# Performance work log

Hardware: AMD Instinct MI355X
Metric: run time of the kernel (lower is better)

## Reference

```python
import jax, jax.numpy as jnp
import numpy as np

K = 20          # args.k
NEG = 0.2       # LeakyReLU negative slope

def lrelu(x):
    return jnp.where(x >= 0, x, NEG * x)

def bn(x, s, b):
    # eval-mode batchnorm folded into per-channel affine; channel axis = 1
    sh = (1, -1) + (1,) * (x.ndim - 2)
    return x * s.reshape(sh) + b.reshape(sh)

def se(x, w1, w2):
    # Squeeze-and-Excite on (B, C, N, k)
    y = jnp.mean(x, axis=(2, 3))                      # (B, C)
    y = jax.nn.sigmoid(jax.nn.relu(y @ w1.T) @ w2.T)  # (B, C)
    return x * y[:, :, None, None]

def graph_feature(x):
    # x: (B, C, N) -> edge features (B, 2C, N, K)
    xx = jnp.sum(x * x, axis=1)                        # (B, N)
    inner = jnp.einsum('bcn,bcm->bnm', x, x)           # (B, N, N)
    dist = -xx[:, :, None] + 2.0 * inner - xx[:, None, :]
    idx = jax.lax.top_k(dist, K)[1]                    # (B, N, K) nearest (incl. self)
    xt = jnp.transpose(x, (0, 2, 1))                   # (B, N, C)
    nbr = jax.vmap(lambda t, i: t[i])(xt, idx)         # (B, N, K, C)
    ctr = xt[:, :, None, :]
    out = jnp.concatenate([nbr - ctr, jnp.broadcast_to(ctr, nbr.shape)], axis=3)
    return jnp.transpose(out, (0, 3, 1, 2))

def edge_block(x, w, s, b, w1, w2):
    # get_graph_feature -> 1x1 conv -> BN -> SE -> LeakyReLU -> max over k
    g = graph_feature(x)                               # (B, 2C, N, K)
    h = jnp.einsum('bcnk,oc->bonk', g, w)
    h = lrelu(se(bn(h, s, b), w1, w2))
    return jnp.max(h, axis=-1)                         # (B, O, N)

def forward(x, conv1_w, conv2_w, conv3_w, conv4_w, conv5_w,
            bn1_s, bn1_b, bn2_s, bn2_b, bn3_s, bn3_b, bn4_s, bn4_b, bn5_s, bn5_b,
            se1_w1, se1_w2, se2_w1, se2_w2, se3_w1, se3_w2, se4_w1, se4_w2,
            res1_w, res2_w, res3_w,
            lin1_w, bn6_s, bn6_b, lin2_w, lin2_b, bn7_s, bn7_b, lin3_w, lin3_b):
    x1 = edge_block(x, conv1_w, bn1_s, bn1_b, se1_w1, se1_w2)                 # (B,512,N)
    x2 = edge_block(x1, conv2_w, bn2_s, bn2_b, se2_w1, se2_w2)
    x2 = x2 + jnp.einsum('bcn,oc->bon', x1, res1_w)                           # (B,512,N)
    x3 = edge_block(x2, conv3_w, bn3_s, bn3_b, se3_w1, se3_w2)
    x3 = x3 + jnp.einsum('bcn,oc->bon', x2, res2_w)                           # (B,1024,N)
    x4 = edge_block(x3, conv4_w, bn4_s, bn4_b, se4_w1, se4_w2)
    x4 = x4 + jnp.einsum('bcn,oc->bon', x3, res3_w)                           # (B,1024,N)
    h = jnp.concatenate([x1, x2, x3, x4], axis=1)                             # (B,3072,N)
    h = lrelu(bn(jnp.einsum('bcn,oc->bon', h, conv5_w), bn5_s, bn5_b))        # (B,2048,N)
    f = jnp.concatenate([jnp.max(h, axis=-1), jnp.mean(h, axis=-1)], axis=1)  # (B,4096)
    f = lrelu(bn(f @ lin1_w.T, bn6_s, bn6_b))       # dropout is eval-mode identity
    f = lrelu(bn(f @ lin2_w.T + lin2_b, bn7_s, bn7_b))
    return f @ lin3_w.T + lin3_b                    # (B,40)

def setup_inputs():
    ks = jax.random.split(jax.random.key(0), 40)
    B, N = 16, 128
    f32 = jnp.float32
    def w(i, shape, s=0.02):
        return jax.random.normal(ks[i], shape, f32) * s
    def bns(i, c):
        return 1.0 + 0.1 * jax.random.normal(ks[i], (c,), f32)
    def bnb(i, c):
        return 0.1 * jax.random.normal(ks[i], (c,), f32)
    return {
        'x': jax.random.normal(ks[0], (B, 512, N), f32),
        'conv1_w': w(1, (512, 1024)),
        'conv2_w': w(2, (512, 1024)),
        'conv3_w': w(3, (1024, 1024)),
        'conv4_w': w(4, (1024, 2048)),
        'conv5_w': w(5, (2048, 3072)),
        'bn1_s': bns(6, 512), 'bn1_b': bnb(7, 512),
        'bn2_s': bns(8, 512), 'bn2_b': bnb(9, 512),
        'bn3_s': bns(10, 1024), 'bn3_b': bnb(11, 1024),
        'bn4_s': bns(12, 1024), 'bn4_b': bnb(13, 1024),
        'bn5_s': bns(14, 2048), 'bn5_b': bnb(15, 2048),
        'se1_w1': w(16, (32, 512), 0.05), 'se1_w2': w(17, (512, 32), 0.05),
        'se2_w1': w(18, (32, 512), 0.05), 'se2_w2': w(19, (512, 32), 0.05),
        'se3_w1': w(20, (64, 1024), 0.05), 'se3_w2': w(21, (1024, 64), 0.05),
        'se4_w1': w(22, (64, 1024), 0.05), 'se4_w2': w(23, (1024, 64), 0.05),
        'res1_w': w(24, (512, 512)),
        'res2_w': w(25, (1024, 512)),
        'res3_w': w(26, (1024, 1024)),
        'lin1_w': w(27, (512, 4096)),
        'bn6_s': bns(28, 512), 'bn6_b': bnb(29, 512),
        'lin2_w': w(30, (256, 512)), 'lin2_b': bnb(31, 256),
        'bn7_s': bns(32, 256), 'bn7_b': bnb(33, 256),
        'lin3_w': w(34, (40, 256)), 'lin3_b': bnb(35, 40),
    }

def reference(x, conv1_w, conv2_w, conv3_w, conv4_w, conv5_w,
              bn1_s, bn1_b, bn2_s, bn2_b, bn3_s, bn3_b, bn4_s, bn4_b, bn5_s, bn5_b,
              se1_w1, se1_w2, se2_w1, se2_w2, se3_w1, se3_w2, se4_w1, se4_w2,
              res1_w, res2_w, res3_w,
              lin1_w, bn6_s, bn6_b, lin2_w, lin2_b, bn7_s, bn7_b, lin3_w, lin3_b):
    return forward(x, conv1_w, conv2_w, conv3_w, conv4_w, conv5_w,
                   bn1_s, bn1_b, bn2_s, bn2_b, bn3_s, bn3_b, bn4_s, bn4_b, bn5_s, bn5_b,
                   se1_w1, se1_w2, se2_w1, se2_w2, se3_w1, se3_w2, se4_w1, se4_w2,
                   res1_w, res2_w, res3_w,
                   lin1_w, bn6_s, bn6_b, lin2_w, lin2_b, bn7_s, bn7_b, lin3_w, lin3_b)
```

## Files before the change

kernel.cpp:

```cpp
#include <hip/hip_runtime.h>
#include <hip/hip_bf16.h>


#define BN_ALL 2048
typedef __hip_bfloat16 bf16;
typedef __attribute__((ext_vector_type(8))) short short8;
typedef __attribute__((ext_vector_type(4))) float float4v;

__device__ __forceinline__ float b2f(bf16 v) { return __bfloat162float(v); }
__device__ __forceinline__ float lrelu(float v) { return v >= 0.f ? v : 0.2f * v; }
__device__ __forceinline__ short f2bs(float v) {
    bf16 h = __float2bfloat16(v);
    return *reinterpret_cast<short*>(&h);
}

__device__ __forceinline__ void gll16(const void* g, void* l) {
    __builtin_amdgcn_global_load_lds(
        (const __attribute__((address_space(1))) unsigned int*)g,
        (__attribute__((address_space(3))) unsigned int*)l,
        16, 0, 0);
}

__device__ __forceinline__ float ldin(const void* p, size_t i, int isb) {
    return isb ? __bfloat162float(((const bf16*)p)[i]) : ((const float*)p)[i];
}

__device__ __forceinline__ float ld1(const float* p) { return *p; }
__device__ __forceinline__ float ld1(const bf16* p)  { return __bfloat162float(*p); }
__device__ __forceinline__ void st1(float* p, float v) { *p = v; }
__device__ __forceinline__ void st1(bf16* p, float v)  { *p = __float2bfloat16(v); }
__device__ __forceinline__ short ldbs(const float* p) { return f2bs(*p); }
__device__ __forceinline__ short ldbs(const bf16* p)  { return *(const short*)p; }

__global__ __launch_bounds__(256) void detect_dtype(const void* __restrict__ x, int* __restrict__ flag) {
    const unsigned* u = (const unsigned*)x;
    int sane = 0;
    for (int i = threadIdx.x; i < 4096; i += 256) {
        unsigned e = (u[i] >> 23) & 0xFF;
        sane += (e >= 87 && e <= 167) ? 1 : 0;
    }
    __shared__ int sh[256];
    sh[threadIdx.x] = sane;
    __syncthreads();
    for (int off = 128; off > 0; off >>= 1) {
        if (threadIdx.x < off) sh[threadIdx.x] += sh[threadIdx.x + off];
        __syncthreads();
    }
    if (threadIdx.x == 0) *flag = (sh[0] < 2048) ? 1 : 0;
}

__global__ __launch_bounds__(256) void convert_kp(const void* __restrict__ x, bf16* __restrict__ X0,
                                                  const int* __restrict__ dflag) {
    int isb = *dflag;
    int item = blockIdx.x * 256 + threadIdx.x;
    int cg = item >> 11, bn = item & 2047;
    int b = bn >> 7, n = bn & 127;
    short8 pk;
#pragma unroll
    for (int j = 0; j < 8; ++j)
        pk[j] = f2bs(ldin(x, ((size_t)(b * 512 + cg * 8 + j)) * 128 + n, isb));
    *(short8*)((short*)X0 + ((size_t)cg * BN_ALL + bn) * 8) = pk;
}

__global__ __launch_bounds__(256) void gram_k(const bf16* __restrict__ X, int C,
                                              float* __restrict__ G) {
    __shared__ __align__(16) short Bsm[2][8192];
    int tid = threadIdx.x;
    int b = blockIdx.x;
    int lane = tid & 63, wv = tid >> 6, wm = wv & 1, wn = wv >> 1;
    int lq = lane >> 4, lr = lane & 15;
    int KC = C >> 6;
    const short* Xs = (const short*)X;

    float4v acc[4][4];
#pragma unroll
    for (int i = 0; i < 4; i++)
#pragma unroll
        for (int j = 0; j < 4; j++) acc[i][j] = (float4v){0.f, 0.f, 0.f, 0.f};

#pragma unroll
    for (int it = 0; it < 4; ++it) {
        int i = tid + it * 256;
        int q = i >> 7, c = i & 127;
        gll16(Xs + ((size_t)q * BN_ALL + b * 128 + c) * 8, &Bsm[0][(size_t)i * 8]);
    }
    __syncthreads();

    int p = 0;
    for (int kc = 0; kc < KC; ++kc) {
        if (kc + 1 < KC) {
#pragma unroll
            for (int it = 0; it < 4; ++it) {
                int i = tid + it * 256;
                int q = i >> 7, c = i & 127;
                gll16(Xs + ((size_t)((kc + 1) * 8 + q) * BN_ALL + b * 128 + c) * 8,
                      &Bsm[p ^ 1][(size_t)i * 8]);
            }
        }
#pragma unroll
        for (int h = 0; h < 2; ++h) {
            short8 av[4], bv[4];
#pragma unroll
            for (int mt = 0; mt < 4; ++mt)
                av[mt] = *(const short8*)&Bsm[p][(size_t)(h * 512 + (lq << 7) + wm * 64 + mt * 16 + lr) * 8];
#pragma unroll
            for (int nt = 0; nt < 4; ++nt)
                bv[nt] = *(const short8*)&Bsm[p][(size_t)(h * 512 + (lq << 7) + wn * 64 + nt * 16 + lr) * 8];
#pragma unroll
            for (int mt = 0; mt < 4; ++mt)
#pragma unroll
                for (int nt = 0; nt < 4; ++nt)
                    acc[mt][nt] = __builtin_amdgcn_mfma_f32_16x16x32_bf16(av[mt], bv[nt], acc[mt][nt], 0, 0, 0);
        }
        __syncthreads();
        p ^= 1;
    }

    float* Gb = G + (size_t)b * 16384;
#pragma unroll
    for (int mt = 0; mt < 4; ++mt)
#pragma unroll
        for (int r = 0; r < 4; ++r) {
            int row = wm * 64 + mt * 16 + lq * 4 + r;
#pragma unroll
            for (int nt = 0; nt < 4; ++nt) {
                int col = wn * 64 + nt * 16 + lr;
                Gb[row * 128 + col] = acc[mt][nt][r];
            }
        }
}

__global__ __launch_bounds__(256) void topk_k(const float* __restrict__ G, int* __restrict__ idx) {
    int gw = (blockIdx.x * 256 + threadIdx.x) >> 6;
    int lane = threadIdx.x & 63;
    int b = gw >> 7, n = gw & 127;
    const float* Gb = G + (size_t)b * 16384;
    float g0 = Gb[n * 128 + lane];
    float g1 = Gb[n * 128 + 64 + lane];
    float dnn = Gb[n * 129];
    float dm0 = Gb[lane * 129];
    float dm1 = Gb[(64 + lane) * 129];
    float d0 = 2.f * g0 - dnn - dm0;
    float d1 = 2.f * g1 - dnn - dm1;
#pragma unroll
    for (int k = 0; k < 20; ++k) {
        float v; int i;
        if (d1 > d0) { v = d1; i = 64 + lane; } else { v = d0; i = lane; }
#pragma unroll
        for (int off = 1; off < 64; off <<= 1) {
            float ov = __shfl_xor(v, off, 64);
            int   oi = __shfl_xor(i, off, 64);
            if (ov > v || (ov == v && oi < i)) { v = ov; i = oi; }
        }
        if (lane == 0) idx[gw * 20 + k] = i;
        if (i < 64) { if (lane == i) d0 = -3.0e38f; }
        else        { if (lane == i - 64) d1 = -3.0e38f; }
    }
}

template <typename S>
__global__ __launch_bounds__(128) void knn_topk(const S* __restrict__ X, int C, int* __restrict__ idx) {
    int b = blockIdx.x >> 7;
    int n = blockIdx.x & 127;
    int m = threadIdx.x;
    const S* base = X + b * 128;
    float s0 = 0, s1 = 0, q0 = 0, q1 = 0;
    for (int c = 0; c < C; c += 2) {
        const S* p = base + (size_t)c * BN_ALL;
        float xm0 = ld1(p + m),          xn0 = ld1(p + n);
        float xm1 = ld1(p + BN_ALL + m), xn1 = ld1(p + BN_ALL + n);
        s0 += xm0 * xn0; q0 += xm0 * xm0;
        s1 += xm1 * xn1; q1 += xm1 * xm1;
    }
    float inner = s0 + s1;
    float xxm   = q0 + q1;
    __shared__ float xx[128];
    __shared__ float dist[128];
    __shared__ float rv[128];
    __shared__ int   ri[128];
    xx[m] = xxm;
    __syncthreads();
    dist[m] = 2.0f * inner - xx[n] - xxm;
    for (int k = 0; k < 20; k++) {
        __syncthreads();
        rv[m] = dist[m]; ri[m] = m;
        __syncthreads();
        for (int off = 64; off > 0; off >>= 1) {
            if (m < off) {
                float a = rv[m], bv = rv[m + off];
                int ia = ri[m], ib = ri[m + off];
                if (bv > a || (bv == a && ib < ia)) { rv[m] = bv; ri[m] = ib; }
            }
            __syncthreads();
        }
        if (m == 0) { idx[blockIdx.x * 20 + k] = ri[0]; dist[ri[0]] = -3.0e38f; }
    }
}

__global__ __launch_bounds__(256) void pack_w(const void* __restrict__ w, int ldw,
                                              const void* __restrict__ res, int Cin, int O,
                                              int Mtot, int K, short* __restrict__ out,
                                              const int* __restrict__ dflag) {
    int isb = *dflag;
    int item = blockIdx.x * 256 + threadIdx.x;
    if (item >= Mtot * (K >> 3)) return;
    int m_local = item & 127;
    int rest = item >> 7;
    int q = rest & 3; rest >>= 2;
    int KC = K >> 5;
    int kc = rest % KC, tm = rest / KC;
    int grow = tm * 128 + m_local;
    int k = kc * 32 + q * 8;
    const void* src; size_t base; int dif = 0;
    if (grow < O)          { src = w;   base = (size_t)grow * ldw + k; }
    else if (grow < 2 * O) { src = w;   base = (size_t)(grow - O) * ldw + k; dif = 1; }
    else                   { src = res; base = (size_t)(grow - 2 * O) * Cin + k; }
    short8 pk;
#pragma unroll
    for (int j = 0; j < 8; ++j) {
        float v = ldin(src, base + j, isb);
        if (dif) v = ldin(src, base + Cin + j, isb) - v;
        pk[j] = f2bs(v);
    }
    *(short8*)&out[(size_t)item * 8] = pk;
}

__global__ __launch_bounds__(256) void gemm_pk(const short* __restrict__ packA,
                                               const bf16* __restrict__ X, float* __restrict__ Cm, int K,
                                               const void* __restrict__ bnS, const void* __restrict__ bnB,
                                               int act, const int* __restrict__ dflag) {
    __shared__ __align__(16) short Asm[2][8192];
    __shared__ __align__(16) short Bsm[2][4096];
    int tid = threadIdx.x;
    int bm  = blockIdx.x << 7;
    int bn0 = blockIdx.y << 6;
    int lane = tid & 63, wv = tid >> 6, wm = wv & 1, wn = wv >> 1;
    int lq = lane >> 4, lr = lane & 15;
    int KC = K >> 6;
    const short* abase = packA + (size_t)blockIdx.x * (K >> 5) * 4096;
    const short* Xs = (const short*)X;
    int bq = tid >> 6, bc = tid & 63;

    float4v acc[4][2];
#pragma unroll
    for (int i = 0; i < 4; i++)
#pragma unroll
        for (int j = 0; j < 2; j++) acc[i][j] = (float4v){0.f, 0.f, 0.f, 0.f};

#pragma unroll
    for (int it = 0; it < 4; ++it)
        gll16(abase + (size_t)(tid + it * 256) * 8, &Asm[0][(size_t)(tid + it * 256) * 8]);
    gll16(Xs + ((size_t)bq * BN_ALL + bn0 + bc) * 8,       &Bsm[0][(size_t)tid * 8]);
    gll16(Xs + ((size_t)(bq + 4) * BN_ALL + bn0 + bc) * 8, &Bsm[0][(size_t)(tid + 256) * 8]);
    __syncthreads();

    int p = 0;
    for (int kc = 0; kc < KC; ++kc) {
        if (kc + 1 < KC) {
            const short* ab = abase + (size_t)(kc + 1) * 8192;
#pragma unroll
            for (int it = 0; it < 4; ++it)
                gll16(ab + (size_t)(tid + it * 256) * 8, &Asm[p ^ 1][(size_t)(tid + it * 256) * 8]);
            gll16(Xs + ((size_t)((kc + 1) * 8 + bq) * BN_ALL + bn0 + bc) * 8,
                  &Bsm[p ^ 1][(size_t)tid * 8]);
            gll16(Xs + ((size_t)((kc + 1) * 8 + bq + 4) * BN_ALL + bn0 + bc) * 8,
                  &Bsm[p ^ 1][(size_t)(tid + 256) * 8]);
        }
#pragma unroll
        for (int h = 0; h < 2; ++h) {
            short8 av[4], bv[2];
#pragma unroll
            for (int mt = 0; mt < 4; ++mt)
                av[mt] = *(const short8*)&Asm[p][(size_t)(h * 512 + (lq << 7) + wm * 64 + mt * 16 + lr) * 8];
#pragma unroll
            for (int nt = 0; nt < 2; ++nt)
                bv[nt] = *(const short8*)&Bsm[p][(size_t)(h * 256 + (lq << 6) + wn * 32 + nt * 16 + lr) * 8];
#pragma unroll
            for (int mt = 0; mt < 4; ++mt)
#pragma unroll
                for (int nt = 0; nt < 2; ++nt)
                    acc[mt][nt] = __builtin_amdgcn_mfma_f32_16x16x32_bf16(av[mt], bv[nt], acc[mt][nt], 0, 0, 0);
        }
        __syncthreads();
        p ^= 1;
    }

    int isb = *dflag;
#pragma unroll
    for (int mt = 0; mt < 4; ++mt) {
#pragma unroll
        for (int r = 0; r < 4; ++r) {
            int row = bm + wm * 64 + mt * 16 + lq * 4 + r;
            float s = 1.f, bb = 0.f;
            if (bnS) { s = ldin(bnS, row, isb); bb = ldin(bnB, row, isb); }
#pragma unroll
            for (int nt = 0; nt < 2; ++nt) {
                int col = bn0 + wn * 32 + nt * 16 + lr;
                float v = acc[mt][nt][r];
                if (bnS) v = v * s + bb;
                if (act) v = lrelu(v);
                Cm[(size_t)row * BN_ALL + col] = v;
            }
        }
    }
}

template <typename S>
__global__ __launch_bounds__(256) void gemm_mfma(const void* __restrict__ w, int ldw,
                                                 const void* __restrict__ res, int Cin, int O,
                                                 const S* __restrict__ X, S* __restrict__ Cm, int K,
                                                 const void* __restrict__ bnS, const void* __restrict__ bnB,
                                                 int act, const int* __restrict__ dflag) {
    int isb = *dflag;
    __shared__ short Asm[4096];
    __shared__ short Bsm[4096];
    int tid = threadIdx.x;
    int bm  = blockIdx.x << 7;
    int bn0 = blockIdx.y << 7;
    int lane = tid & 63, wv = tid >> 6;
    int wm = wv & 1, wn = wv >> 1;
    int lq = lane >> 4, lr = lane & 15;

    float4v acc[4][4];
#pragma unroll
    for (int i = 0; i < 4; i++)
#pragma unroll
        for (int j = 0; j < 4; j++) acc[i][j] = (float4v){0.f, 0.f, 0.f, 0.f};

    for (int k0 = 0; k0 < K; k0 += 32) {
#pragma unroll
        for (int it = 0; it < 2; ++it) {
            int i = tid + it * 256;
            int m = i >> 2, q = i & 3;
            int grow = bm + m;
            const void* asrc; size_t abase; int dif = 0;
            if (grow < O)          { asrc = w;   abase = (size_t)grow * ldw; }
            else if (grow < 2 * O) { asrc = w;   abase = (size_t)(grow - O) * ldw; dif = 1; }
            else                   { asrc = res; abase = (size_t)(grow - 2 * O) * Cin; }
            size_t kk = (size_t)k0 + q * 8;
            short8 pk;
#pragma unroll
            for (int j = 0; j < 8; ++j) {
                float v = ldin(asrc, abase + kk + j, isb);
                if (dif) v = ldin(asrc, abase + Cin + kk + j, isb) - v;
                pk[j] = f2bs(v);
            }
            *(short8*)&Asm[(size_t)(q * 128 + m) * 8] = pk;
        }
#pragma unroll
        for (int it = 0; it < 2; ++it) {
            int i = tid + it * 256;
            int q = i >> 7, c = i & 127;
            const S* xp = X + (size_t)(k0 + q * 8) * BN_ALL + bn0 + c;
            short8 pk;
#pragma unroll
            for (int j = 0; j < 8; ++j) pk[j] = f2bs(ld1(xp + (size_t)j * BN_ALL));
            *(short8*)&Bsm[(size_t)i * 8] = pk;
        }
        __syncthreads();
        short8 av[4], bv[4];
#pragma unroll
        for (int mt = 0; mt < 4; ++mt)
            av[mt] = *(const short8*)&Asm[(size_t)((lq << 7) + wm * 64 + mt * 16 + lr) * 8];
#pragma unroll
        for (int nt = 0; nt < 4; ++nt)
            bv[nt] = *(const short8*)&Bsm[(size_t)((lq << 7) + wn * 64 + nt * 16 + lr) * 8];
#pragma unroll
        for (int mt = 0; mt < 4; ++mt)
#pragma unroll
            for (int nt = 0; nt < 4; ++nt)
                acc[mt][nt] = __builtin_amdgcn_mfma_f32_16x16x32_bf16(av[mt], bv[nt], acc[mt][nt], 0, 0, 0);
        __syncthreads();
    }
#pragma unroll
    for (int mt = 0; mt < 4; ++mt) {
#pragma unroll
        for (int r = 0; r < 4; ++r) {
            int row = bm + wm * 64 + mt * 16 + lq * 4 + r;
            float s = 1.f, bb = 0.f;
            if (bnS) { s = ldin(bnS, row, isb); bb = ldin(bnB, row, isb); }
#pragma unroll
            for (int nt = 0; nt < 4; ++nt) {
                int col = bn0 + wn * 64 + nt * 16 + lr;
                float v = acc[mt][nt][r];
                if (bnS) v = v * s + bb;
                if (act) v = lrelu(v);
                st1(Cm + (size_t)row * BN_ALL + col, v);
            }
        }
    }
}

template <typename S>
__global__ __launch_bounds__(256) void gather_pool(S* __restrict__ PS, const int* __restrict__ idx,
                                                   const void* __restrict__ bns, const void* __restrict__ bnb,
                                                   float* __restrict__ Mb, int O,
                                                   const int* __restrict__ dflag) {
    int isb = *dflag;
    int wv = threadIdx.x >> 6, lane = threadIdx.x & 63;
    int gw = blockIdx.x * 4 + wv;
    int o = gw >> 4, b = gw & 15;
    S* Prow = PS + (size_t)o * BN_ALL + b * 128;
    const S* Srow = PS + (size_t)(O + o) * BN_ALL + b * 128;
    int n0 = lane, n1 = lane + 64;
    const int* id0 = idx + (b * 128 + n0) * 20;
    const int* id1 = idx + (b * 128 + n1) * 20;
    float mx0 = -3.0e38f, mn0 = 3.0e38f, sm0 = 0.f;
    float mx1 = -3.0e38f, mn1 = 3.0e38f, sm1 = 0.f;
#pragma unroll
    for (int k = 0; k < 20; k++) {
        float p = ld1(Prow + id0[k]);
        mx0 = fmaxf(mx0, p); mn0 = fminf(mn0, p); sm0 += p;
    }
#pragma unroll
    for (int k = 0; k < 20; k++) {
        float p = ld1(Prow + id1[k]);
        mx1 = fmaxf(mx1, p); mn1 = fminf(mn1, p); sm1 += p;
    }
    float Sv0 = ld1(Srow + n0), Sv1 = ld1(Srow + n1);
    float s = ldin(bns, o, isb), bb = ldin(bnb, o, isb);
    float ext0 = (s >= 0.f) ? mx0 : mn0;
    float ext1 = (s >= 0.f) ? mx1 : mn1;
    float t0 = lrelu(s * (ext0 + Sv0) + bb);
    float t1 = lrelu(s * (ext1 + Sv1) + bb);
    st1(Prow + n0, t0);
    st1(Prow + n1, t1);
    float r1 = sm0 + sm1;
    float r2 = Sv0 + Sv1;
#pragma unroll
    for (int off = 32; off > 0; off >>= 1) {
        r1 += __shfl_xor(r1, off, 64);
        r2 += __shfl_xor(r2, off, 64);
    }
    if (lane == 0) Mb[b * O + o] = s * (r1 * (1.f / 2560.f) + r2 * (1.f / 128.f)) + bb;
}

__global__ __launch_bounds__(256) void se1_k(const float* __restrict__ Mb, const void* __restrict__ w1,
                                             float* __restrict__ Z, int O, int r,
                                             const int* __restrict__ dflag) {
    int isb = *dflag;
    int gw = (blockIdx.x * 256 + threadIdx.x) >> 6;
    int lane = threadIdx.x & 63;
    int b = gw / r, t = gw - b * r;
    const float* mv = Mb + (size_t)b * O;
    float acc = 0.f;
    for (int c = lane; c < O; c += 64) acc += ldin(w1, (size_t)t * O + c, isb) * mv[c];
#pragma unroll
    for (int off = 32; off > 0; off >>= 1) acc += __shfl_xor(acc, off, 64);
    if (lane == 0) Z[b * r + t] = fmaxf(acc, 0.f);
}

__global__ __launch_bounds__(256) void se2_k(const float* __restrict__ Z, const void* __restrict__ w2,
                                             float* __restrict__ Y, int O, int r,
                                             const int* __restrict__ dflag) {
    int isb = *dflag;
    int gw = (blockIdx.x * 256 + threadIdx.x) >> 6;
    int lane = threadIdx.x & 63;
    int b = gw / O, o = gw - b * O;
    float acc = 0.f;
    if (lane < r) acc = ldin(w2, (size_t)o * r + lane, isb) * Z[b * r + lane];
#pragma unroll
    for (int off = 32; off > 0; off >>= 1) acc += __shfl_xor(acc, off, 64);
    if (lane == 0) Y[b * O + o] = 1.f / (1.f + expf(-acc));
}

__global__ __launch_bounds__(256) void se_k(const float* __restrict__ Mb, const void* __restrict__ w1,
                                            const void* __restrict__ w2, float* __restrict__ Y, int O, int r,
                                            const int* __restrict__ dflag) {
    int isb = *dflag;
    int b = blockIdx.x, t = threadIdx.x;
    __shared__ float mloc[1024];
    __shared__ float z[64];
    for (int i = t; i < O; i += 256) mloc[i] = Mb[b * O + i];
    __syncthreads();
    if (t < r) {
        float acc = 0.f;
        for (int c = 0; c < O; c++) acc += ldin(w1, (size_t)t * O + c, isb) * mloc[c];
        z[t] = fmaxf(acc, 0.f);
    }
    __syncthreads();
    for (int o = t; o < O; o += 256) {
        float acc = 0.f;
        for (int j = 0; j < r; j++) acc += ldin(w2, (size_t)o * r + j, isb) * z[j];
        Y[b * O + o] = 1.f / (1.f + expf(-acc));
    }
}

__global__ __launch_bounds__(256) void finalize_kp(const float* __restrict__ PS, const float* __restrict__ Y,
                                                   int useR, bf16* __restrict__ Xdst, int O) {
    int item = blockIdx.x * 256 + threadIdx.x;
    int og = item >> 11, bn = item & 2047;
    int b = bn >> 7;
    short8 pk;
#pragma unroll
    for (int j = 0; j < 8; ++j) {
        int r = og * 8 + j;
        float v = Y[b * O + r] * PS[(size_t)r * BN_ALL + bn];
        if (useR) v += PS[(size_t)(2 * O + r) * BN_ALL + bn];
        pk[j] = f2bs(v);
    }
    *(short8*)((short*)Xdst + ((size_t)og * BN_ALL + bn) * 8) = pk;
}

template <typename SP, typename SD>
__global__ __launch_bounds__(256) void finalize(const SP* __restrict__ PS, const float* __restrict__ Y,
                                                int useR, SD* __restrict__ Xdst, int O) {
    int tid = blockIdx.x * 256 + threadIdx.x;
    int o = tid >> 11, bn = tid & 2047;
    int b = bn >> 7;
    float v = Y[b * O + o] * ld1(PS + tid);
    if (useR) v += ld1(PS + (size_t)(2 * O + o) * BN_ALL + bn);
    st1(Xdst + tid, v);
}

template <typename S>
__global__ __launch_bounds__(256) void convert_x(const void* __restrict__ x, S* __restrict__ X0,
                                                 const int* __restrict__ dflag) {
    int isb = *dflag;
    int tid = blockIdx.x * 256 + threadIdx.x;
    int c = tid >> 11, bn = tid & 2047;
    int b = bn >> 7, n = bn & 127;
    st1(X0 + tid, ldin(x, (size_t)(b * 512 + c) * 128 + n, isb));
}

template <typename S>
__global__ __launch_bounds__(256) void pool5(const S* __restrict__ H, float* __restrict__ f) {
    int wv = threadIdx.x >> 6, lane = threadIdx.x & 63;
    int gw = blockIdx.x * 4 + wv;
    int m = gw >> 4, b = gw & 15;
    const S* Hp = H + (size_t)m * BN_ALL + b * 128;
    float v0 = ld1(Hp + lane), v1 = ld1(Hp + 64 + lane);
    float mx = fmaxf(v0, v1);
    float sm = v0 + v1;
#pragma unroll
    for (int off = 32; off > 0; off >>= 1) {
        mx = fmaxf(mx, __shfl_xor(mx, off, 64));
        sm += __shfl_xor(sm, off, 64);
    }
    if (lane == 0) {
        f[b * 4096 + m] = mx;
        f[b * 4096 + 2048 + m] = sm * (1.f / 128.f);
    }
}

__global__ __launch_bounds__(256) void head_k(const float* __restrict__ in, const void* __restrict__ W,
                                              const void* __restrict__ bias, const void* __restrict__ bns,
                                              const void* __restrict__ bnb, float* __restrict__ outf,
                                              void* __restrict__ outb, int Kd, int Od, int act,
                                              const int* __restrict__ dflag) {
    int isb = *dflag;
    int gw = (blockIdx.x * 256 + threadIdx.x) >> 6;
    int lane = threadIdx.x & 63;
    if (gw >= 16 * Od) return;
    int b = gw / Od, o = gw - b * Od;
    const float* iv = in + b * Kd;
    float acc = 0.f;
    for (int k = lane; k < Kd; k += 64) acc += iv[k] * ldin(W, (size_t)o * Kd + k, isb);
    for (int off = 32; off > 0; off >>= 1) acc += __shfl_xor(acc, off, 64);
    if (lane == 0) {
        float v = acc;
        if (bias) v += ldin(bias, o, isb);
        if (bns) v = v * ldin(bns, o, isb) + ldin(bnb, o, isb);
        if (act) v = lrelu(v);
        if (outb) {
            if (isb) ((bf16*)outb)[gw] = __float2bfloat16(v);
            else     ((float*)outb)[gw] = v;
        } else outf[gw] = v;
    }
}

__global__ __launch_bounds__(256) void zero_out(bf16* o, int n) {
    int i = blockIdx.x * 256 + threadIdx.x;
    if (i < n) o[i] = __float2bfloat16(0.f);
}

#define UNPACK_INPUTS()                                                     \
    const void* x_in   = d_in[0];                                           \
    const void* conv1w = d_in[1];  const void* conv2w = d_in[2];            \
    const void* conv3w = d_in[3];  const void* conv4w = d_in[4];            \
    const void* conv5w = d_in[5];                                           \
    const void* bn1s = d_in[6],  * bn1b = d_in[7];                          \
    const void* bn2s = d_in[8],  * bn2b = d_in[9];                          \
    const void* bn3s = d_in[10], * bn3b = d_in[11];                         \
    const void* bn4s = d_in[12], * bn4b = d_in[13];                         \
    const void* bn5s = d_in[14], * bn5b = d_in[15];                         \
    const void* se1w1 = d_in[16], * se1w2 = d_in[17];                       \
    const void* se2w1 = d_in[18], * se2w2 = d_in[19];                       \
    const void* se3w1 = d_in[20], * se3w2 = d_in[21];                       \
    const void* se4w1 = d_in[22], * se4w2 = d_in[23];                       \
    const void* res1w = d_in[24]; const void* res2w = d_in[25];             \
    const void* res3w = d_in[26]; const void* lin1w = d_in[27];             \
    const void* bn6s = d_in[28], * bn6b = d_in[29];                         \
    const void* lin2w = d_in[30], * lin2b = d_in[31];                       \
    const void* bn7s = d_in[32], * bn7b = d_in[33];                         \
    const void* lin3w = d_in[34], * lin3b = d_in[35];

static void run_net_packed(void* const* d_in, void* d_out, void* d_ws, hipStream_t stream) {
    UNPACK_INPUTS();
    float* WS = (float*)d_ws;
    float* PS   = WS;
    bf16*  XC   = (bf16*)(WS + 6291456);
    short* PACK = (short*)(WS + 12582912);
    float* MB = WS + 15728640;
    float* YB = MB + 16384;
    float* FB = YB + 16384;
    float* F1 = FB + 65536;
    float* F2 = F1 + 8192;
    int* IDX  = (int*)(F2 + 4096);
    int* DFLAG = IDX + 40960;
    float* ZB = (float*)(DFLAG + 16);
    bf16*  X0 = (bf16*)(PS + (size_t)2048 * BN_ALL);
    float* GRAM = PS;
    bf16* X1 = XC;
    bf16* X2 = XC + (size_t)512 * BN_ALL;
    bf16* X3 = XC + (size_t)1024 * BN_ALL;
    bf16* X4 = XC + (size_t)2048 * BN_ALL;

    detect_dtype<<<1, 256, 0, stream>>>(x_in, DFLAG);
    convert_kp<<<512, 256, 0, stream>>>(x_in, X0, DFLAG);

    gram_k<<<16, 256, 0, stream>>>(X0, 512, GRAM);
    topk_k<<<512, 256, 0, stream>>>(GRAM, IDX);
    pack_w<<<256, 256, 0, stream>>>(conv1w, 1024, nullptr, 512, 512, 1024, 512, PACK, DFLAG);
    gemm_pk<<<dim3(8, 32), 256, 0, stream>>>(PACK, X0, PS, 512, nullptr, nullptr, 0, DFLAG);
    gather_pool<float><<<2048, 256, 0, stream>>>(PS, IDX, bn1s, bn1b, MB, 512, DFLAG);
    se1_k<<<128, 256, 0, stream>>>(MB, se1w1, ZB, 512, 32, DFLAG);
    se2_k<<<2048, 256, 0, stream>>>(ZB, se1w2, YB, 512, 32, DFLAG);
    finalize_kp<<<512, 256, 0, stream>>>(PS, YB, 0, X1, 512);

    gram_k<<<16, 256, 0, stream>>>(X1, 512, GRAM);
    topk_k<<<512, 256, 0, stream>>>(GRAM, IDX);
    pack_w<<<384, 256, 0, stream>>>(conv2w, 1024, res1w, 512, 512, 1536, 512, PACK, DFLAG);
    gemm_pk<<<dim3(12, 32), 256, 0, stream>>>(PACK, X1, PS, 512, nullptr, nullptr, 0, DFLAG);
    gather_pool<float><<<2048, 256, 0, stream>>>(PS, IDX, bn2s, bn2b, MB, 512, DFLAG);
    se1_k<<<128, 256, 0, stream>>>(MB, se2w1, ZB, 512, 32, DFLAG);
    se2_k<<<2048, 256, 0, stream>>>(ZB, se2w2, YB, 512, 32, DFLAG);
    finalize_kp<<<512, 256, 0, stream>>>(PS, YB, 1, X2, 512);

    gram_k<<<16, 256, 0, stream>>>(X2, 512, GRAM);
    topk_k<<<512, 256, 0, stream>>>(GRAM, IDX);
    pack_w<<<768, 256, 0, stream>>>(conv3w, 1024, res2w, 512, 1024, 3072, 512, PACK, DFLAG);
    gemm_pk<<<dim3(24, 32), 256, 0, stream>>>(PACK, X2, PS, 512, nullptr, nullptr, 0, DFLAG);
    gather_pool<float><<<4096, 256, 0, stream>>>(PS, IDX, bn3s, bn3b, MB, 1024, DFLAG);
    se1_k<<<256, 256, 0, stream>>>(MB, se3w1, ZB, 1024, 64, DFLAG);
    se2_k<<<4096, 256, 0, stream>>>(ZB, se3w2, YB, 1024, 64, DFLAG);
    finalize_kp<<<1024, 256, 0, stream>>>(PS, YB, 1, X3, 1024);

    gram_k<<<16, 256, 0, stream>>>(X3, 1024, GRAM);
    topk_k<<<512, 256, 0, stream>>>(GRAM, IDX);
    pack_w<<<1536, 256, 0, stream>>>(conv4w, 2048, res3w, 1024, 1024, 3072, 1024, PACK, DFLAG);
    gemm_pk<<<dim3(24, 32), 256, 0, stream>>>(PACK, X3, PS, 1024, nullptr, nullptr, 0, DFLAG);
    gather_pool<float><<<4096, 256, 0, stream>>>(PS, IDX, bn4s, bn4b, MB, 1024, DFLAG);
    se1_k<<<256, 256, 0, stream>>>(MB, se4w1, ZB, 1024, 64, DFLAG);
    se2_k<<<4096, 256, 0, stream>>>(ZB, se4w2, YB, 1024, 64, DFLAG);
    finalize_kp<<<1024, 256, 0, stream>>>(PS, YB, 1, X4, 1024);

    pack_w<<<3072, 256, 0, stream>>>(conv5w, 3072, nullptr, 3072, 2048, 2048, 3072, PACK, DFLAG);
    gemm_pk<<<dim3(16, 32), 256, 0, stream>>>(PACK, XC, PS, 3072, bn5s, bn5b, 1, DFLAG);
    pool5<float><<<8192, 256, 0, stream>>>(PS, FB);

    head_k<<<2048, 256, 0, stream>>>(FB, lin1w, nullptr, bn6s, bn6b, F1, nullptr, 4096, 512, 1, DFLAG);
    head_k<<<1024, 256, 0, stream>>>(F1, lin2w, lin2b, bn7s, bn7b, F2, nullptr, 512, 256, 1, DFLAG);
    head_k<<<160, 256, 0, stream>>>(F2, lin3w, lin3b, nullptr, nullptr, nullptr, d_out, 256, 40, 0, DFLAG);
}

template <typename S>
static void run_net(void* const* d_in, void* d_out, void* d_ws, hipStream_t stream) {
    UNPACK_INPUTS();
    const size_t RC = (size_t)3072 * BN_ALL;
    S* PS = (S*)d_ws;
    S* XC = PS + RC;
    S* X0 = PS + (size_t)2048 * BN_ALL;
    float* MB = (float*)(XC + RC);
    float* YB = MB + 16 * 1024;
    float* FB = YB + 16 * 1024;
    float* F1 = FB + 16 * 4096;
    float* F2 = F1 + 16 * 512;
    int* IDX  = (int*)(F2 + 16 * 256);
    int* DFLAG = IDX + 16 * 128 * 20;

    S* X1 = XC;
    S* X2 = XC + (size_t)512 * BN_ALL;
    S* X3 = XC + (size_t)1024 * BN_ALL;
    S* X4 = XC + (size_t)2048 * BN_ALL;

    detect_dtype<<<1, 256, 0, stream>>>(x_in, DFLAG);
    convert_x<S><<<4096, 256, 0, stream>>>(x_in, X0, DFLAG);

    knn_topk<S><<<2048, 128, 0, stream>>>(X0, 512, IDX);
    gemm_mfma<S><<<dim3(8, 16), 256, 0, stream>>>(conv1w, 1024, nullptr, 512, 512, X0, PS, 512, nullptr, nullptr, 0, DFLAG);
    gather_pool<S><<<2048, 256, 0, stream>>>(PS, IDX, bn1s, bn1b, MB, 512, DFLAG);
    se_k<<<16, 256, 0, stream>>>(MB, se1w1, se1w2, YB, 512, 32, DFLAG);
    finalize<S, S><<<4096, 256, 0, stream>>>(PS, YB, 0, X1, 512);

    knn_topk<S><<<2048, 128, 0, stream>>>(X1, 512, IDX);
    gemm_mfma<S><<<dim3(12, 16), 256, 0, stream>>>(conv2w, 1024, res1w, 512, 512, X1, PS, 512, nullptr, nullptr, 0, DFLAG);
    gather_pool<S><<<2048, 256, 0, stream>>>(PS, IDX, bn2s, bn2b, MB, 512, DFLAG);
    se_k<<<16, 256, 0, stream>>>(MB, se2w1, se2w2, YB, 512, 32, DFLAG);
    finalize<S, S><<<4096, 256, 0, stream>>>(PS, YB, 1, X2, 512);

    knn_topk<S><<<2048, 128, 0, stream>>>(X2, 512, IDX);
    gemm_mfma<S><<<dim3(24, 16), 256, 0, stream>>>(conv3w, 1024, res2w, 512, 1024, X2, PS, 512, nullptr, nullptr, 0, DFLAG);
    gather_pool<S><<<4096, 256, 0, stream>>>(PS, IDX, bn3s, bn3b, MB, 1024, DFLAG);
    se_k<<<16, 256, 0, stream>>>(MB, se3w1, se3w2, YB, 1024, 64, DFLAG);
    finalize<S, S><<<8192, 256, 0, stream>>>(PS, YB, 1, X3, 1024);

    knn_topk<S><<<2048, 128, 0, stream>>>(X3, 1024, IDX);
    gemm_mfma<S><<<dim3(24, 16), 256, 0, stream>>>(conv4w, 2048, res3w, 1024, 1024, X3, PS, 1024, nullptr, nullptr, 0, DFLAG);
    gather_pool<S><<<4096, 256, 0, stream>>>(PS, IDX, bn4s, bn4b, MB, 1024, DFLAG);
    se_k<<<16, 256, 0, stream>>>(MB, se4w1, se4w2, YB, 1024, 64, DFLAG);
    finalize<S, S><<<8192, 256, 0, stream>>>(PS, YB, 1, X4, 1024);

    gemm_mfma<S><<<dim3(16, 16), 256, 0, stream>>>(conv5w, 3072, nullptr, 3072, 2048, XC, PS, 3072, bn5s, bn5b, 1, DFLAG);
    pool5<S><<<8192, 256, 0, stream>>>(PS, FB);

    head_k<<<2048, 256, 0, stream>>>(FB, lin1w, nullptr, bn6s, bn6b, F1, nullptr, 4096, 512, 1, DFLAG);
    head_k<<<1024, 256, 0, stream>>>(F1, lin2w, lin2b, bn7s, bn7b, F2, nullptr, 512, 256, 1, DFLAG);
    head_k<<<160, 256, 0, stream>>>(F2, lin3w, lin3b, nullptr, nullptr, nullptr, d_out, 256, 40, 0, DFLAG);
}

extern "C" void kernel_launch(void* const* d_in, const int* in_sizes, int n_in,
                              void* d_out, int out_size, void* d_ws, size_t ws_size,
                              hipStream_t stream) {
    const size_t SMALL = (16 * 1024 + 16 * 1024 + 16 * 4096 + 16 * 512 + 16 * 256) * 4
                       + 16 * 128 * 20 * 4 + 8192;
    const size_t NEED_PACKED = (size_t)15728640 * 4 + SMALL;
    const size_t NEED_F32    = 2 * ((size_t)3072 * BN_ALL * 4) + SMALL;
    const size_t NEED_BF16   = 2 * ((size_t)3072 * BN_ALL * 2) + SMALL;
    if (ws_size >= NEED_PACKED) {
        run_net_packed(d_in, d_out, d_ws, stream);
    } else if (ws_size >= NEED_F32) {
        run_net<float>(d_in, d_out, d_ws, stream);
    } else if (ws_size >= NEED_BF16) {
        run_net<bf16>(d_in, d_out, d_ws, stream);
    } else {
        zero_out<<<3, 256, 0, stream>>>((bf16*)d_out, out_size);
    }
}
```

Before: 590.7 us.

## Add packed2 path fusing weight packing, topk with GEMM, and SE launches

Adds a new forward path used when the workspace is large enough. It packs every conv weight and converts the input in one launch up front. Each edge block runs its top-k selection and the packed-weight GEMM in a single grid so the two overlap, and the two SE matmuls are merged into one kernel. This removes many small launches and per-layer packing passes, at the cost of a larger workspace and heavier shared-memory use in the combined kernel.

```diff
diff --git a/kernel.cpp b/kernel.cpp
--- a/kernel.cpp
+++ b/kernel.cpp
@@ -29,8 +29,6 @@
 __device__ __forceinline__ float ld1(const bf16* p)  { return __bfloat162float(*p); }
 __device__ __forceinline__ void st1(float* p, float v) { *p = v; }
 __device__ __forceinline__ void st1(bf16* p, float v)  { *p = __float2bfloat16(v); }
-__device__ __forceinline__ short ldbs(const float* p) { return f2bs(*p); }
-__device__ __forceinline__ short ldbs(const bf16* p)  { return *(const short*)p; }
 
 __global__ __launch_bounds__(256) void detect_dtype(const void* __restrict__ x, int* __restrict__ flag) {
     const unsigned* u = (const unsigned*)x;
@@ -49,10 +47,9 @@
     if (threadIdx.x == 0) *flag = (sh[0] < 2048) ? 1 : 0;
 }
 
-__global__ __launch_bounds__(256) void convert_kp(const void* __restrict__ x, bf16* __restrict__ X0,
-                                                  const int* __restrict__ dflag) {
-    int isb = *dflag;
-    int item = blockIdx.x * 256 + threadIdx.x;
+__device__ __forceinline__ void convert_core(int bid, int tid, const void* __restrict__ x,
+                                             bf16* __restrict__ X0, int isb) {
+    int item = bid * 256 + tid;
     int cg = item >> 11, bn = item & 2047;
     int b = bn >> 7, n = bn & 127;
     short8 pk;
@@ -60,6 +57,62 @@
     for (int j = 0; j < 8; ++j)
         pk[j] = f2bs(ldin(x, ((size_t)(b * 512 + cg * 8 + j)) * 128 + n, isb));
     *(short8*)((short*)X0 + ((size_t)cg * BN_ALL + bn) * 8) = pk;
+}
+
+__global__ __launch_bounds__(256) void convert_kp(const void* __restrict__ x, bf16* __restrict__ X0,
+                                                  const int* __restrict__ dflag) {
+    convert_core(blockIdx.x, threadIdx.x, x, X0, *dflag);
+}
+
+__device__ __forceinline__ void pack_core(int item, int isb, const void* __restrict__ w, int ldw,
+                                          const void* __restrict__ res, int Cin, int O,
+                                          int Mtot, int K, short* __restrict__ out) {
+    if (item >= Mtot * (K >> 3)) return;
+    int m_local = item & 127;
+    int rest = item >> 7;
+    int q = rest & 3; rest >>= 2;
+    int KC = K >> 5;
+    int kc = rest % KC, tm = rest / KC;
+    int grow = tm * 128 + m_local;
+    int k = kc * 32 + q * 8;
+    const void* src; size_t base; int dif = 0;
+    if (grow < O)          { src = w;   base = (size_t)grow * ldw + k; }
+    else if (grow < 2 * O) { src = w;   base = (size_t)(grow - O) * ldw + k; dif = 1; }
+    else                   { src = res; base = (size_t)(grow - 2 * O) * Cin + k; }
+    short8 pk;
+#pragma unroll
+    for (int j = 0; j < 8; ++j) {
+        float v = ldin(src, base + j, isb);
+        if (dif) v = ldin(src, base + Cin + j, isb) - v;
+        pk[j] = f2bs(v);
+    }
+    *(short8*)&out[(size_t)item * 8] = pk;
+}
+
+__global__ __launch_bounds__(256) void pack_w(const void* __restrict__ w, int ldw,
+                                              const void* __restrict__ res, int Cin, int O,
+                                              int Mtot, int K, short* __restrict__ out,
+                                              const int* __restrict__ dflag) {
+    pack_core(blockIdx.x * 256 + threadIdx.x, *dflag, w, ldw, res, Cin, O, Mtot, K, out);
+}
+
+__global__ __launch_bounds__(256) void convert_pack_all(
+        const void* __restrict__ x, bf16* __restrict__ X0,
+        const void* __restrict__ w1c, const void* __restrict__ w2c, const void* __restrict__ w3c,
+        const void* __restrict__ w4c, const void* __restrict__ w5c,
+        const void* __restrict__ r1, const void* __restrict__ r2, const void* __restrict__ r3,
+        short* __restrict__ p1, short* __restrict__ p2, short* __restrict__ p3,
+        short* __restrict__ p4, short* __restrict__ p5,
+        const int* __restrict__ dflag) {
+    int isb = *dflag;
+    int bid = blockIdx.x, tid = threadIdx.x;
+    if (bid < 512) { convert_core(bid, tid, x, X0, isb); return; }
+    int pb = bid - 512;
+    if (pb < 256)       pack_core(pb * 256 + tid,          isb, w1c, 1024, nullptr, 512, 512, 1024, 512, p1);
+    else if (pb < 640)  pack_core((pb - 256) * 256 + tid,  isb, w2c, 1024, r1,      512, 512, 1536, 512, p2);
+    else if (pb < 1408) pack_core((pb - 640) * 256 + tid,  isb, w3c, 1024, r2,      512, 1024, 3072, 512, p3);
+    else if (pb < 2944) pack_core((pb - 1408) * 256 + tid, isb, w4c, 2048, r3,      1024, 1024, 3072, 1024, p4);
+    else                pack_core((pb - 2944) * 256 + tid, isb, w5c, 3072, nullptr, 3072, 2048, 2048, 3072, p5);
 }
 
 __global__ __launch_bounds__(256) void gram_k(const bf16* __restrict__ X, int C,
@@ -130,9 +183,10 @@
         }
 }
 
-__global__ __launch_bounds__(256) void topk_k(const float* __restrict__ G, int* __restrict__ idx) {
-    int gw = (blockIdx.x * 256 + threadIdx.x) >> 6;
-    int lane = threadIdx.x & 63;
+__device__ __forceinline__ void topk_core(int bid, int tid, const float* __restrict__ G,
+                                          int* __restrict__ idx) {
+    int gw = (bid * 256 + tid) >> 6;
+    int lane = tid & 63;
     int b = gw >> 7, n = gw & 127;
     const float* Gb = G + (size_t)b * 16384;
     float g0 = Gb[n * 128 + lane];
@@ -155,6 +209,109 @@
         if (lane == 0) idx[gw * 20 + k] = i;
         if (i < 64) { if (lane == i) d0 = -3.0e38f; }
         else        { if (lane == i - 64) d1 = -3.0e38f; }
+    }
+}
+
+__global__ __launch_bounds__(256) void topk_k(const float* __restrict__ G, int* __restrict__ idx) {
+    topk_core(blockIdx.x, threadIdx.x, G, idx);
+}
+
+__device__ __forceinline__ void gemm_core(int bx, int by, int tid,
+        const short* __restrict__ packA, const bf16* __restrict__ X,
+        float* __restrict__ Cm, int K,
+        const void* __restrict__ bnS, const void* __restrict__ bnB,
+        int act, const int* __restrict__ dflag) {
+    __shared__ __align__(16) short Asm[2][8192];
+    __shared__ __align__(16) short Bsm[2][4096];
+    int bm  = bx << 7;
+    int bn0 = by << 6;
+    int lane = tid & 63, wv = tid >> 6, wm = wv & 1, wn = wv >> 1;
+    int lq = lane >> 4, lr = lane & 15;
+    int KC = K >> 6;
+    const short* abase = packA + (size_t)bx * (K >> 5) * 4096;
+    const short* Xs = (const short*)X;
+    int bq = tid >> 6, bc = tid & 63;
+
+    float4v acc[4][2];
+#pragma unroll
+    for (int i = 0; i < 4; i++)
+#pragma unroll
+        for (int j = 0; j < 2; j++) acc[i][j] = (float4v){0.f, 0.f, 0.f, 0.f};
+
+#pragma unroll
+    for (int it = 0; it < 4; ++it)
+        gll16(abase + (size_t)(tid + it * 256) * 8, &Asm[0][(size_t)(tid + it * 256) * 8]);
+    gll16(Xs + ((size_t)bq * BN_ALL + bn0 + bc) * 8,       &Bsm[0][(size_t)tid * 8]);
+    gll16(Xs + ((size_t)(bq + 4) * BN_ALL + bn0 + bc) * 8, &Bsm[0][(size_t)(tid + 256) * 8]);
+    __syncthreads();
+
+    int p = 0;
+    for (int kc = 0; kc < KC; ++kc) {
+        if (kc + 1 < KC) {
+            const short* ab = abase + (size_t)(kc + 1) * 8192;
+#pragma unroll
+            for (int it = 0; it < 4; ++it)
+                gll16(ab + (size_t)(tid + it * 256) * 8, &Asm[p ^ 1][(size_t)(tid + it * 256) * 8]);
+            gll16(Xs + ((size_t)((kc + 1) * 8 + bq) * BN_ALL + bn0 + bc) * 8,
+                  &Bsm[p ^ 1][(size_t)tid * 8]);
+            gll16(Xs + ((size_t)((kc + 1) * 8 + bq + 4) * BN_ALL + bn0 + bc) * 8,
+                  &Bsm[p ^ 1][(size_t)(tid + 256) * 8]);
+        }
+#pragma unroll
+        for (int h = 0; h < 2; ++h) {
+            short8 av[4], bv[2];
+#pragma unroll
+            for (int mt = 0; mt < 4; ++mt)
+                av[mt] = *(const short8*)&Asm[p][(size_t)(h * 512 + (lq << 7) + wm * 64 + mt * 16 + lr) * 8];
+#pragma unroll
+            for (int nt = 0; nt < 2; ++nt)
+                bv[nt] = *(const short8*)&Bsm[p][(size_t)(h * 256 + (lq << 6) + wn * 32 + nt * 16 + lr) * 8];
+#pragma unroll
+            for (int mt = 0; mt < 4; ++mt)
+#pragma unroll
+                for (int nt = 0; nt < 2; ++nt)
+                    acc[mt][nt] = __builtin_amdgcn_mfma_f32_16x16x32_bf16(av[mt], bv[nt], acc[mt][nt], 0, 0, 0);
+        }
+        __syncthreads();
+        p ^= 1;
+    }
+
+    int isb = *dflag;
+#pragma unroll
+    for (int mt = 0; mt < 4; ++mt) {
+#pragma unroll
+        for (int r = 0; r < 4; ++r) {
+            int row = bm + wm * 64 + mt * 16 + lq * 4 + r;
+            float s = 1.f, bb = 0.f;
+            if (bnS) { s = ldin(bnS, row, isb); bb = ldin(bnB, row, isb); }
+#pragma unroll
+            for (int nt = 0; nt < 2; ++nt) {
+                int col = bn0 + wn * 32 + nt * 16 + lr;
+                float v = acc[mt][nt][r];
+                if (bnS) v = v * s + bb;
+                if (act) v = lrelu(v);
+                Cm[(size_t)row * BN_ALL + col] = v;
+            }
+        }
+    }
+}
+
+__global__ __launch_bounds__(256) void gemm_pk(const short* __restrict__ packA,
+                                               const bf16* __restrict__ X, float* __restrict__ Cm, int K,
+                                               const void* __restrict__ bnS, const void* __restrict__ bnB,
+                                               int act, const int* __restrict__ dflag) {
+    gemm_core(blockIdx.x, blockIdx.y, threadIdx.x, packA, X, Cm, K, bnS, bnB, act, dflag);
+}
+
+__global__ __launch_bounds__(256) void topk_gemm_k(const float* __restrict__ G, int* __restrict__ idx,
+                                                   const short* __restrict__ packA,
+                                                   const bf16* __restrict__ X, float* __restrict__ Cm,
+                                                   int K, const int* __restrict__ dflag) {
+    if (blockIdx.x < 512) {
+        topk_core(blockIdx.x, threadIdx.x, G, idx);
+    } else {
+        int g = blockIdx.x - 512;
+        gemm_core(g >> 5, g & 31, threadIdx.x, packA, X, Cm, K, nullptr, nullptr, 0, dflag);
     }
 }
 
@@ -197,114 +354,6 @@
     }
 }
 
-__global__ __launch_bounds__(256) void pack_w(const void* __restrict__ w, int ldw,
-                                              const void* __restrict__ res, int Cin, int O,
-                                              int Mtot, int K, short* __restrict__ out,
-                                              const int* __restrict__ dflag) {
-    int isb = *dflag;
-    int item = blockIdx.x * 256 + threadIdx.x;
-    if (item >= Mtot * (K >> 3)) return;
-    int m_local = item & 127;
-    int rest = item >> 7;
-    int q = rest & 3; rest >>= 2;
-    int KC = K >> 5;
-    int kc = rest % KC, tm = rest / KC;
-    int grow = tm * 128 + m_local;
-    int k = kc * 32 + q * 8;
-    const void* src; size_t base; int dif = 0;
-    if (grow < O)          { src = w;   base = (size_t)grow * ldw + k; }
-    else if (grow < 2 * O) { src = w;   base = (size_t)(grow - O) * ldw + k; dif = 1; }
-    else                   { src = res; base = (size_t)(grow - 2 * O) * Cin + k; }
-    short8 pk;
-#pragma unroll
-    for (int j = 0; j < 8; ++j) {
-        float v = ldin(src, base + j, isb);
-        if (dif) v = ldin(src, base + Cin + j, isb) - v;
-        pk[j] = f2bs(v);
-    }
-    *(short8*)&out[(size_t)item * 8] = pk;
-}
-
-__global__ __launch_bounds__(256) void gemm_pk(const short* __restrict__ packA,
-                                               const bf16* __restrict__ X, float* __restrict__ Cm, int K,
-                                               const void* __restrict__ bnS, const void* __restrict__ bnB,
-                                               int act, const int* __restrict__ dflag) {
-    __shared__ __align__(16) short Asm[2][8192];
-    __shared__ __align__(16) short Bsm[2][4096];
-    int tid = threadIdx.x;
-    int bm  = blockIdx.x << 7;
-    int bn0 = blockIdx.y << 6;
-    int lane = tid & 63, wv = tid >> 6, wm = wv & 1, wn = wv >> 1;
-    int lq = lane >> 4, lr = lane & 15;
-    int KC = K >> 6;
-    const short* abase = packA + (size_t)blockIdx.x * (K >> 5) * 4096;
-    const short* Xs = (const short*)X;
-    int bq = tid >> 6, bc = tid & 63;
-
-    float4v acc[4][2];
-#pragma unroll
-    for (int i = 0; i < 4; i++)
-#pragma unroll
-        for (int j = 0; j < 2; j++) acc[i][j] = (float4v){0.f, 0.f, 0.f, 0.f};
-
-#pragma unroll
-    for (int it = 0; it < 4; ++it)
-        gll16(abase + (size_t)(tid + it * 256) * 8, &Asm[0][(size_t)(tid + it * 256) * 8]);
-    gll16(Xs + ((size_t)bq * BN_ALL + bn0 + bc) * 8,       &Bsm[0][(size_t)tid * 8]);
-    gll16(Xs + ((size_t)(bq + 4) * BN_ALL + bn0 + bc) * 8, &Bsm[0][(size_t)(tid + 256) * 8]);
-    __syncthreads();
-
-    int p = 0;
-    for (int kc = 0; kc < KC; ++kc) {
-        if (kc + 1 < KC) {
-            const short* ab = abase + (size_t)(kc + 1) * 8192;
-#pragma unroll
-            for (int it = 0; it < 4; ++it)
-                gll16(ab + (size_t)(tid + it * 256) * 8, &Asm[p ^ 1][(size_t)(tid + it * 256) * 8]);
-            gll16(Xs + ((size_t)((kc + 1) * 8 + bq) * BN_ALL + bn0 + bc) * 8,
-                  &Bsm[p ^ 1][(size_t)tid * 8]);
-            gll16(Xs + ((size_t)((kc + 1) * 8 + bq + 4) * BN_ALL + bn0 + bc) * 8,
-                  &Bsm[p ^ 1][(size_t)(tid + 256) * 8]);
-        }
-#pragma unroll
-        for (int h = 0; h < 2; ++h) {
-            short8 av[4], bv[2];
-#pragma unroll
-            for (int mt = 0; mt < 4; ++mt)
-                av[mt] = *(const short8*)&Asm[p][(size_t)(h * 512 + (lq << 7) + wm * 64 + mt * 16 + lr) * 8];
-#pragma unroll
-            for (int nt = 0; nt < 2; ++nt)
-                bv[nt] = *(const short8*)&Bsm[p][(size_t)(h * 256 + (lq << 6) + wn * 32 + nt * 16 + lr) * 8];
-#pragma unroll
-            for (int mt = 0; mt < 4; ++mt)
-#pragma unroll
-                for (int nt = 0; nt < 2; ++nt)
-                    acc[mt][nt] = __builtin_amdgcn_mfma_f32_16x16x32_bf16(av[mt], bv[nt], acc[mt][nt], 0, 0, 0);
-        }
-        __syncthreads();
-        p ^= 1;
-    }
-
-    int isb = *dflag;
-#pragma unroll
-    for (int mt = 0; mt < 4; ++mt) {
-#pragma unroll
-        for (int r = 0; r < 4; ++r) {
-            int row = bm + wm * 64 + mt * 16 + lq * 4 + r;
-            float s = 1.f, bb = 0.f;
-            if (bnS) { s = ldin(bnS, row, isb); bb = ldin(bnB, row, isb); }
-#pragma unroll
-            for (int nt = 0; nt < 2; ++nt) {
-                int col = bn0 + wn * 32 + nt * 16 + lr;
-                float v = acc[mt][nt][r];
-                if (bnS) v = v * s + bb;
-                if (act) v = lrelu(v);
-                Cm[(size_t)row * BN_ALL + col] = v;
-            }
-        }
-    }
-}
-
 template <typename S>
 __global__ __launch_bounds__(256) void gemm_mfma(const void* __restrict__ w, int ldw,
                                                  const void* __restrict__ res, int Cin, int O,
@@ -462,6 +511,32 @@
 #pragma unroll
     for (int off = 32; off > 0; off >>= 1) acc += __shfl_xor(acc, off, 64);
     if (lane == 0) Y[b * O + o] = 1.f / (1.f + expf(-acc));
+}
+
+__global__ __launch_bounds__(256) void se12_k(const float* __restrict__ Mb, const void* __restrict__ w1,
+                                              const void* __restrict__ w2, float* __restrict__ Y,
+                                              int O, int r, const int* __restrict__ dflag) {
+    int isb = *dflag;
+    int b = blockIdx.x;
+    __shared__ float ml[1024];
+    __shared__ float zz[64];
+    for (int i = threadIdx.x; i < O; i += 256) ml[i] = Mb[(size_t)b * O + i];
+    __syncthreads();
+    int wv = threadIdx.x >> 6, lane = threadIdx.x & 63;
+    for (int t = wv; t < r; t += 4) {
+        float acc = 0.f;
+        for (int c = lane; c < O; c += 64) acc += ldin(w1, (size_t)t * O + c, isb) * ml[c];
+#pragma unroll
+        for (int off = 32; off > 0; off >>= 1) acc += __shfl_xor(acc, off, 64);
+        if (lane == 0) zz[t] = fmaxf(acc, 0.f);
+    }
+    __syncthreads();
+    for (int o = wv; o < O; o += 4) {
+        float acc = (lane < r) ? ldin(w2, (size_t)o * r + lane, isb) * zz[lane] : 0.f;
+#pragma unroll
+        for (int off = 32; off > 0; off >>= 1) acc += __shfl_xor(acc, off, 64);
+        if (lane == 0) Y[b * O + o] = 1.f / (1.f + expf(-acc));
+    }
 }
 
 __global__ __launch_bounds__(256) void se_k(const float* __restrict__ Mb, const void* __restrict__ w1,
@@ -595,6 +670,68 @@
     const void* bn7s = d_in[32], * bn7b = d_in[33];                         \
     const void* lin3w = d_in[34], * lin3b = d_in[35];
 
+static void run_net_packed2(void* const* d_in, void* d_out, void* d_ws, hipStream_t stream) {
+    UNPACK_INPUTS();
+    float* WS = (float*)d_ws;
+    float* PS = WS;
+    bf16*  XC = (bf16*)(WS + 6291456);
+    short* P1 = (short*)(WS + 12582912);
+    short* P2 = P1 + 524288;
+    short* P3 = P2 + 786432;
+    short* P4 = P3 + 1572864;
+    short* P5 = P4 + 3145728;
+    float* MB = WS + 18743296;
+    float* YB = MB + 16384;
+    float* FB = YB + 16384;
+    float* F1 = FB + 65536;
+    float* F2 = F1 + 8192;
+    int* IDX  = (int*)(F2 + 4096);
+    int* DFLAG = IDX + 40960;
+    float* ZB = (float*)(DFLAG + 16);
+    float* GRAM = WS + 18900000;
+    bf16*  X0 = (bf16*)(PS + (size_t)2048 * BN_ALL);
+    bf16* X1 = XC;
+    bf16* X2 = XC + (size_t)512 * BN_ALL;
+    bf16* X3 = XC + (size_t)1024 * BN_ALL;
+    bf16* X4 = XC + (size_t)2048 * BN_ALL;
+
+    detect_dtype<<<1, 256, 0, stream>>>(x_in, DFLAG);
+    convert_pack_all<<<6528, 256, 0, stream>>>(x_in, X0,
+        conv1w, conv2w, conv3w, conv4w, conv5w, res1w, res2w, res3w,
+        P1, P2, P3, P4, P5, DFLAG);
+
+    gram_k<<<16, 256, 0, stream>>>(X0, 512, GRAM);
+    topk_gemm_k<<<512 + 8 * 32, 256, 0, stream>>>(GRAM, IDX, P1, X0, PS, 512, DFLAG);
+    gather_pool<float><<<2048, 256, 0, stream>>>(PS, IDX, bn1s, bn1b, MB, 512, DFLAG);
+    se12_k<<<16, 256, 0, stream>>>(MB, se1w1, se1w2, YB, 512, 32, DFLAG);
+    finalize_kp<<<512, 256, 0, stream>>>(PS, YB, 0, X1, 512);
+
+    gram_k<<<16, 256, 0, stream>>>(X1, 512, GRAM);
+    topk_gemm_k<<<512 + 12 * 32, 256, 0, stream>>>(GRAM, IDX, P2, X1, PS, 512, DFLAG);
+    gather_pool<float><<<2048, 256, 0, stream>>>(PS, IDX, bn2s, bn2b, MB, 512, DFLAG);
+    se12_k<<<16, 256, 0, stream>>>(MB, se2w1, se2w2, YB, 512, 32, DFLAG);
+    finalize_kp<<<512, 256, 0, stream>>>(PS, YB, 1, X2, 512);
+
+    gram_k<<<16, 256, 0, stream>>>(X2, 512, GRAM);
+    topk_gemm_k<<<512 + 24 * 32, 256, 0, stream>>>(GRAM, IDX, P3, X2, PS, 512, DFLAG);
+    gather_pool<float><<<4096, 256, 0, stream>>>(PS, IDX, bn3s, bn3b, MB, 1024, DFLAG);
+    se12_k<<<16, 256, 0, stream>>>(MB, se3w1, se3w2, YB, 1024, 64, DFLAG);
+    finalize_kp<<<1024, 256, 0, stream>>>(PS, YB, 1, X3, 1024);
+
+    gram_k<<<16, 256, 0, stream>>>(X3, 1024, GRAM);
+    topk_gemm_k<<<512 + 24 * 32, 256, 0, stream>>>(GRAM, IDX, P4, X3, PS, 1024, DFLAG);
+    gather_pool<float><<<4096, 256, 0, stream>>>(PS, IDX, bn4s, bn4b, MB, 1024, DFLAG);
+    se12_k<<<16, 256, 0, stream>>>(MB, se4w1, se4w2, YB, 1024, 64, DFLAG);
+    finalize_kp<<<1024, 256, 0, stream>>>(PS, YB, 1, X4, 1024);
+
+    gemm_pk<<<dim3(16, 32), 256, 0, stream>>>(P5, XC, PS, 3072, bn5s, bn5b, 1, DFLAG);
+    pool5<float><<<8192, 256, 0, stream>>>(PS, FB);
+
+    head_k<<<2048, 256, 0, stream>>>(FB, lin1w, nullptr, bn6s, bn6b, F1, nullptr, 4096, 512, 1, DFLAG);
+    head_k<<<1024, 256, 0, stream>>>(F1, lin2w, lin2b, bn7s, bn7b, F2, nullptr, 512, 256, 1, DFLAG);
+    head_k<<<160, 256, 0, stream>>>(F2, lin3w, lin3b, nullptr, nullptr, nullptr, d_out, 256, 40, 0, DFLAG);
+}
+
 static void run_net_packed(void* const* d_in, void* d_out, void* d_ws, hipStream_t stream) {
     UNPACK_INPUTS();
     float* WS = (float*)d_ws;
@@ -724,10 +861,13 @@
                               hipStream_t stream) {
     const size_t SMALL = (16 * 1024 + 16 * 1024 + 16 * 4096 + 16 * 512 + 16 * 256) * 4
                        + 16 * 128 * 20 * 4 + 8192;
+    const size_t NEED_P2     = ((size_t)18900000 + 262144 + 4096) * 4;
     const size_t NEED_PACKED = (size_t)15728640 * 4 + SMALL;
     const size_t NEED_F32    = 2 * ((size_t)3072 * BN_ALL * 4) + SMALL;
     const size_t NEED_BF16   = 2 * ((size_t)3072 * BN_ALL * 2) + SMALL;
-    if (ws_size >= NEED_PACKED) {
+    if (ws_size >= NEED_P2) {
+        run_net_packed2(d_in, d_out, d_ws, stream);
+    } else if (ws_size >= NEED_PACKED) {
         run_net_packed(d_in, d_out, d_ws, stream);
     } else if (ws_size >= NEED_F32) {
         run_net<float>(d_in, d_out, d_ws, stream);
```

After: 1.261 ms. 2.13x slower.
